# Kernel optimization log

Measured on AMD Instinct MI355X. Metric: run time of the kernel, lower is better.

The kernel has to match this reference:

```python
import jax, jax.numpy as jnp
import numpy as np

B, D = 4096, 1024
N_CLASSES = 100
INF = jnp.float32(3.4e38)


def setup_inputs() -> dict:
    key = jax.random.key(0)
    k1, k2 = jax.random.split(key)
    x = jax.random.normal(k1, (B, 1, D), dtype=jnp.float32)
    labels = jax.random.randint(k2, (B,), 0, N_CLASSES)
    return {"x": x, "labels": labels}


def _awareness_scan(xs, labels_f, R_init):
    # xs: [B, D] float32, labels_f: [B] float32
    b, d = xs.shape
    slots = jnp.arange(b)

    def step(state, inp):
        refs, ref_labels, n_refs, count, min_d, max_d, R = state
        xi, li = inp
        mask = slots < n_refs  # active reference slots
        # distances from candidate to current reference set (torch.cdist, p=2)
        d_all = jnp.sqrt(jnp.sum((refs - xi[None, :]) ** 2, axis=-1))  # [B]
        d_all = jax.lax.stop_gradient(d_all)
        d_act = jnp.where(mask, d_all, INF)
        min_act = jnp.min(d_act)
        is_first = count == 1
        # new reference iff ALL active distances exceed R (i.e. min > R)
        insert = is_first | (min_act > R)
        refs2 = jnp.where(insert, refs.at[n_refs].set(xi), refs)
        ref_labels2 = jnp.where(insert, ref_labels.at[n_refs].set(li), ref_labels)
        n_refs2 = n_refs + insert.astype(n_refs.dtype)
        # dynamic ray update (skipped on the very first sample, as in torch)
        max_act = jnp.max(jnp.where(mask, d_all, -INF))
        min_d2 = jnp.where(is_first, min_d, jnp.minimum(min_d, min_act))
        max_d2 = jnp.where(is_first, max_d, jnp.maximum(max_d, max_act))
        R2 = jnp.where(is_first, R, (min_d2 + max_d2) / 3)
        # prediction: nearest reference AFTER potential insertion
        mask2 = slots < n_refs2
        d2 = jnp.sqrt(jnp.sum((refs2 - xi[None, :]) ** 2, axis=-1))
        d2 = jax.lax.stop_gradient(d2)
        idx = jnp.argmin(jnp.where(mask2, d2, INF))
        pred = ref_labels2[idx]
        new_state = (refs2, ref_labels2, n_refs2, count + 1, min_d2, max_d2, R2)
        return new_state, pred

    init = (
        jnp.zeros((b, d), jnp.float32),   # reference instances buffer
        jnp.zeros((b,), jnp.float32),     # reference labels buffer
        jnp.int32(0),                     # n_refs
        jnp.int32(1),                     # count (starts at 1, as in torch)
        INF,                              # min_dist
        jnp.float32(0.0),                 # max_dist
        jnp.float32(R_init),              # R
    )
    _, preds = jax.lax.scan(step, init, (xs, labels_f))
    return preds  # [B] float32


def reference(x, labels):
    # x: [B, 1, D]; labels: [B] int. update_ref_insts=True, set_labels=labels.
    xs = x.reshape(x.shape[0], x.shape[2])
    labels_f = labels.astype(jnp.float32)
    return _awareness_scan(xs, labels_f, 1.0)
```

## Files before the change

### kernel.cpp

```cpp
#include <hip/hip_runtime.h>
#include <stdint.h>

#define B_N   4096
#define D_DIM 1024
#define INF_F 3.4e38f

typedef float floatx4 __attribute__((ext_vector_type(4)));

#define XQ_OFF 131072

__global__ __launch_bounds__(256)
void k_prep(const float* __restrict__ x, unsigned char* __restrict__ xq,
            float* __restrict__ norms,
            unsigned long long* __restrict__ minpack,
            unsigned int* __restrict__ maxbits) {
    const int row = blockIdx.x;
    const int t   = threadIdx.x;
    float4 v = ((const float4*)x)[row * 256 + t];
    int p = __builtin_amdgcn_cvt_pk_fp8_f32(v.x, v.y, 0, false);
    p     = __builtin_amdgcn_cvt_pk_fp8_f32(v.z, v.w, p, true);
    ((int*)xq)[row * 256 + t] = p;
    float s = v.x * v.x + v.y * v.y + v.z * v.z + v.w * v.w;
    #pragma unroll
    for (int off = 32; off; off >>= 1) s += __shfl_down(s, off);
    __shared__ float ws4[4];
    if ((t & 63) == 0) ws4[t >> 6] = s;
    __syncthreads();
    if (t == 0) {
        norms[row]   = ws4[0] + ws4[1] + ws4[2] + ws4[3];
        minpack[row] = 0xFFFFFFFFFFFFFFFFull;
        maxbits[row] = 0u;
    }
}

#define GLDS(g, l)                                                              \
    __builtin_amdgcn_global_load_lds(                                           \
        (__attribute__((address_space(1))) void*)(void*)(g),                    \
        (__attribute__((address_space(3))) void*)(void*)(l), 16, 0, 0)

__global__ __launch_bounds__(256, 3)
void k_pass1_fp8(const unsigned char* __restrict__ xq,
                 const float* __restrict__ norms,
                 unsigned long long* __restrict__ minpack,
                 unsigned int* __restrict__ maxbits) {
    int bid = blockIdx.x;
    int ti  = (int)((sqrtf(8.f * bid + 1.f) - 1.f) * 0.5f);
    while ((ti + 1) * (ti + 2) / 2 <= bid) ti++;
    while (ti * (ti + 1) / 2 > bid) ti--;
    int tj  = bid - ti * (ti + 1) / 2;

    __shared__ unsigned char As[16384];
    __shared__ unsigned char Bs[16384];
    __shared__ unsigned long long redMin[128][2];
    __shared__ float redMax[128][2];

    const int t    = threadIdx.x;
    const int w    = t >> 6, lane = t & 63;
    const int wm   = w >> 1, wn = w & 1;
    const int q4   = lane >> 4, c15 = lane & 15;
    const int i0   = ti * 128, j0 = tj * 128;

    const int sr = lane >> 3;
    const int sc = (lane & 7) ^ (sr & 7);

    const unsigned char* gA[4]; const unsigned char* gB[4];
    unsigned char* lA[4]; unsigned char* lB[4];
    #pragma unroll
    for (int q = 0; q < 4; q++) {
        int e   = w * 4 + q;
        int row = e * 8 + sr;
        gA[q] = xq + (size_t)(i0 + row) * D_DIM + sc * 16;
        gB[q] = xq + (size_t)(j0 + row) * D_DIM + sc * 16;
        lA[q] = As + e * 1024;
        lB[q] = Bs + e * 1024;
    }

    const int r7 = c15 & 7;
    int oib[4];
    #pragma unroll
    for (int kk = 0; kk < 4; kk++) {
        int sl  = kk * 2 + (q4 >> 1);
        oib[kk] = (((sl ^ r7) << 4) | ((q4 & 1) << 3));
    }
    int rbA[4], rbB[4];
    #pragma unroll
    for (int st = 0; st < 4; st++) {
        rbA[st] = (wm * 64 + st * 16 + c15) * 128;
        rbB[st] = (wn * 64 + st * 16 + c15) * 128;
    }

    floatx4 acc[4][4];
    #pragma unroll
    for (int m = 0; m < 4; m++)
        #pragma unroll
        for (int n = 0; n < 4; n++)
            acc[m][n] = (floatx4){0.f, 0.f, 0.f, 0.f};

    for (int it = 0; it < 8; it++) {
        __syncthreads();
        #pragma unroll
        for (int q = 0; q < 4; q++) {
            GLDS(gA[q], lA[q]);
            GLDS(gB[q], lB[q]);
            gA[q] += 128; gB[q] += 128;
        }
        __syncthreads();
        #pragma unroll
        for (int kk = 0; kk < 4; kk++) {
            long long af[4], bfr[4];
            #pragma unroll
            for (int st = 0; st < 4; st++) {
                af[st]  = *(const long long*)(As + rbA[st] + oib[kk]);
                bfr[st] = *(const long long*)(Bs + rbB[st] + oib[kk]);
            }
            #pragma unroll
            for (int m = 0; m < 4; m++)
                #pragma unroll
                for (int n = 0; n < 4; n++)
                    acc[m][n] = __builtin_amdgcn_mfma_f32_16x16x32_fp8_fp8(
                        af[m], bfr[n], acc[m][n], 0, 0, 0);
        }
    }

    float nj[4];
    #pragma unroll
    for (int st = 0; st < 4; st++) nj[st] = norms[j0 + wn * 64 + st * 16 + c15];

    #pragma unroll
    for (int st_m = 0; st_m < 4; st_m++) {
        #pragma unroll
        for (int r = 0; r < 4; r++) {
            int i_loc = wm * 64 + st_m * 16 + q4 * 4 + r;
            int gi    = i0 + i_loc;
            float ni  = norms[gi];
            unsigned long long mp = 0xFFFFFFFFFFFFFFFFull;
            float mx = -INF_F;
            #pragma unroll
            for (int st_n = 0; st_n < 4; st_n++) {
                int gj = j0 + wn * 64 + st_n * 16 + c15;
                if (gj < gi) {
                    float dot = acc[st_m][st_n][r];
                    float d   = sqrtf(fmaxf(ni + nj[st_n] - 2.f * dot, 0.f));
                    unsigned long long p =
                        ((unsigned long long)__float_as_uint(d) << 32) | (unsigned)gj;
                    if (p < mp) mp = p;
                    mx = fmaxf(mx, d);
                }
            }
            #pragma unroll
            for (int off = 1; off < 16; off <<= 1) {
                unsigned long long op = __shfl_xor(mp, off, 64);
                if (op < mp) mp = op;
                float om = __shfl_xor(mx, off, 64);
                mx = fmaxf(mx, om);
            }
            if (c15 == 0) { redMin[i_loc][wn] = mp; redMax[i_loc][wn] = mx; }
        }
    }
    __syncthreads();
    if (t < 128) {
        unsigned long long mp = redMin[t][0];
        if (redMin[t][1] < mp) mp = redMin[t][1];
        float mx = fmaxf(redMax[t][0], redMax[t][1]);
        if (mp != 0xFFFFFFFFFFFFFFFFull) {
            atomicMin(&minpack[i0 + t], mp);
            atomicMax(&maxbits[i0 + t], __float_as_uint(mx));
        }
    }
}

__global__ __launch_bounds__(1024)
void k_tail(const unsigned long long* __restrict__ minpack,
            const unsigned int* __restrict__ maxbits,
            const float* __restrict__ x, const float* __restrict__ norms,
            const int* __restrict__ labels, int* __restrict__ ref_idx,
            float* __restrict__ out) {
    const int t = threadIdx.x;
    float m[4], M[4];
    #pragma unroll
    for (int q = 0; q < 4; q++) {
        int i = t * 4 + q;
        unsigned long long p = minpack[i];
        float dmin = (p == 0xFFFFFFFFFFFFFFFFull)
                       ? INF_F : __uint_as_float((unsigned)(p >> 32));
        m[q] = (i == 0) ? INF_F : dmin;
        M[q] = (i == 0) ? -INF_F : __uint_as_float(maxbits[i]);
    }
    float pmin[4], pmax[4];
    pmin[0] = m[0]; pmax[0] = M[0];
    #pragma unroll
    for (int q = 1; q < 4; q++) {
        pmin[q] = fminf(pmin[q - 1], m[q]);
        pmax[q] = fmaxf(pmax[q - 1], M[q]);
    }
    __shared__ float smin[1024], smax[1024];
    smin[t] = pmin[3]; smax[t] = pmax[3];
    __syncthreads();
    for (int off = 1; off < 1024; off <<= 1) {
        float a = (t >= off) ? smin[t - off] : INF_F;
        float b = (t >= off) ? smax[t - off] : -INF_F;
        __syncthreads();
        smin[t] = fminf(smin[t], a);
        smax[t] = fmaxf(smax[t], b);
        __syncthreads();
    }
    float exMin = (t > 0) ? smin[t - 1] : INF_F;
    float exMax = (t > 0) ? smax[t - 1] : -INF_F;

    int viol = B_N;
    #pragma unroll
    for (int q = 0; q < 4; q++) {
        int i = t * 4 + q;
        if (i >= 1) {
            float pm = (q == 0) ? exMin : fminf(exMin, pmin[q - 1]);
            float pM = (q == 0) ? exMax : fmaxf(exMax, pmax[q - 1]);
            float R  = (i == 1) ? 1.0f : (pm + pM) / 3.0f;
            if (!(m[q] > R) && i < viol) viol = i;
        }
    }
    __shared__ int sv[1024];
    sv[t] = viol;
    __syncthreads();
    for (int off = 512; off; off >>= 1) {
        if (t < off) sv[t] = min(sv[t], sv[t + off]);
        __syncthreads();
    }
    const int s_star = sv[0];

    for (int i = t; i < s_star; i += 1024) out[i] = (float)labels[i];

    __shared__ float s_state[3];
    __shared__ int s_n;
    if (s_star < B_N && t == (s_star >> 2)) {
        int q = s_star & 3;
        float pm = (q == 0) ? exMin : fminf(exMin, pmin[q - 1]);
        float pM = (q == 0) ? exMax : fmaxf(exMax, pmax[q - 1]);
        float md = fminf(pm, m[q]);
        float Md = fmaxf(pM, M[q]);
        s_state[0] = md; s_state[1] = Md; s_state[2] = (md + Md) / 3.0f;
        s_n = s_star;
        unsigned long long p = minpack[s_star];
        int j = (int)(unsigned)(p & 0xFFFFFFFFu);
        out[s_star] = (float)labels[j];
    }
    if (s_star >= B_N) return;

    for (int s = t; s < s_star; s += 1024) ref_idx[s] = s;
    __syncthreads();

    __shared__ unsigned long long redp[1024];
    __shared__ float redm[1024];
    for (int i = s_star + 1; i < B_N; i++) {
        int n = s_n;
        const float* xi = x + (size_t)i * D_DIM;
        float ni = norms[i];
        unsigned long long mp = 0xFFFFFFFFFFFFFFFFull;
        float mx = -INF_F;
        for (int slot = t; slot < n; slot += 1024) {
            int j = ref_idx[slot];
            const float* xj = x + (size_t)j * D_DIM;
            float dot = 0.f;
            for (int k = 0; k < D_DIM; k++) dot = fmaf(xi[k], xj[k], dot);
            float d = sqrtf(fmaxf(ni + norms[j] - 2.f * dot, 0.f));
            unsigned long long p =
                ((unsigned long long)__float_as_uint(d) << 32) | (unsigned)slot;
            if (p < mp) mp = p;
            mx = fmaxf(mx, d);
        }
        redp[t] = mp; redm[t] = mx;
        __syncthreads();
        for (int off = 512; off; off >>= 1) {
            if (t < off) {
                if (redp[t + off] < redp[t]) redp[t] = redp[t + off];
                redm[t] = fmaxf(redm[t], redm[t + off]);
            }
            __syncthreads();
        }
        if (t == 0) {
            unsigned long long p = redp[0];
            float min_act = __uint_as_float((unsigned)(p >> 32));
            int minslot   = (int)(unsigned)(p & 0xFFFFFFFFu);
            float max_act = redm[0];
            bool insert = (min_act > s_state[2]);
            int pred;
            if (insert) {
                ref_idx[n] = i;
                s_n = n + 1;
                pred = (min_act <= 0.0f) ? labels[ref_idx[minslot]] : labels[i];
            } else {
                pred = labels[ref_idx[minslot]];
            }
            float md = fminf(s_state[0], min_act);
            float Md = fmaxf(s_state[1], max_act);
            s_state[0] = md; s_state[1] = Md; s_state[2] = (md + Md) / 3.0f;
            out[i] = (float)pred;
        }
        __syncthreads();
    }
}

extern "C" void kernel_launch(void* const* d_in, const int* in_sizes, int n_in,
                              void* d_out, int out_size, void* d_ws, size_t ws_size,
                              hipStream_t stream) {
    const float* x      = (const float*)d_in[0];
    const int*   labels = (const int*)d_in[1];
    float*       out    = (float*)d_out;
    char* ws = (char*)d_ws;
    unsigned long long* minpack = (unsigned long long*)ws;
    unsigned int*       maxbits = (unsigned int*)(ws + 32768);
    float*              norms   = (float*)(ws + 49152);
    int*                ref_idx = (int*)(ws + 65600);
    unsigned char*      xq      = (unsigned char*)(ws + XQ_OFF);

    k_prep<<<B_N, 256, 0, stream>>>(x, xq, norms, minpack, maxbits);
    const int ntiles  = B_N / 128;
    const int nblocks = ntiles * (ntiles + 1) / 2;
    k_pass1_fp8<<<nblocks, 256, 0, stream>>>(xq, norms, minpack, maxbits);
    k_tail<<<1, 1024, 0, stream>>>(minpack, maxbits, x, norms, labels, ref_idx, out);
}
```

Before: 102.3 us.

## Use 64x64 triangular tiles with split-K across two waves and LDS reduction

Shrinks the pairwise-distance GEMM tile from 128x128 with 4 waves to 64x64 with 2 waves, each wave computing half of the K dimension. Partial accumulators are then summed through LDS, and wave 0 does the epilogue with direct atomics. Each wave owns a private LDS region, so the per-iteration block barriers are replaced by a vmcnt wait. This gives about four times as many blocks for better CU occupancy and load balance. In exchange, each block reuses loaded data less and issues more global atomics.

```diff
diff --git a/kernel.cpp b/kernel.cpp
--- a/kernel.cpp
+++ b/kernel.cpp
@@ -4,6 +4,8 @@
 #define B_N   4096
 #define D_DIM 1024
 #define INF_F 3.4e38f
+#define NT    64
+#define NBLK  (NT * (NT + 1) / 2)
 
 typedef float floatx4 __attribute__((ext_vector_type(4)));
 
@@ -38,56 +40,47 @@
         (__attribute__((address_space(1))) void*)(void*)(g),                    \
         (__attribute__((address_space(3))) void*)(void*)(l), 16, 0, 0)
 
-__global__ __launch_bounds__(256, 3)
-void k_pass1_fp8(const unsigned char* __restrict__ xq,
-                 const float* __restrict__ norms,
-                 unsigned long long* __restrict__ minpack,
-                 unsigned int* __restrict__ maxbits) {
+__global__ __launch_bounds__(128, 3)
+void k_pass1(const unsigned char* __restrict__ xq,
+             const float* __restrict__ norms,
+             unsigned long long* __restrict__ minpack,
+             unsigned int* __restrict__ maxbits) {
     int bid = blockIdx.x;
     int ti  = (int)((sqrtf(8.f * bid + 1.f) - 1.f) * 0.5f);
     while ((ti + 1) * (ti + 2) / 2 <= bid) ti++;
     while (ti * (ti + 1) / 2 > bid) ti--;
     int tj  = bid - ti * (ti + 1) / 2;
 
-    __shared__ unsigned char As[16384];
-    __shared__ unsigned char Bs[16384];
-    __shared__ unsigned long long redMin[128][2];
-    __shared__ float redMax[128][2];
+    __shared__ __align__(16) unsigned char lds[16384];
 
     const int t    = threadIdx.x;
     const int w    = t >> 6, lane = t & 63;
-    const int wm   = w >> 1, wn = w & 1;
     const int q4   = lane >> 4, c15 = lane & 15;
-    const int i0   = ti * 128, j0 = tj * 128;
-
-    const int sr = lane >> 3;
-    const int sc = (lane & 7) ^ (sr & 7);
+    const int i0   = ti * 64, j0 = tj * 64;
+
+    unsigned char* myA = lds + w * 8192;
+    unsigned char* myB = myA + 4096;
+
+    const int sr = lane >> 2;
+    const int sc = (lane & 3) ^ (sr & 3);
 
     const unsigned char* gA[4]; const unsigned char* gB[4];
-    unsigned char* lA[4]; unsigned char* lB[4];
-    #pragma unroll
-    for (int q = 0; q < 4; q++) {
-        int e   = w * 4 + q;
-        int row = e * 8 + sr;
-        gA[q] = xq + (size_t)(i0 + row) * D_DIM + sc * 16;
-        gB[q] = xq + (size_t)(j0 + row) * D_DIM + sc * 16;
-        lA[q] = As + e * 1024;
-        lB[q] = Bs + e * 1024;
-    }
-
-    const int r7 = c15 & 7;
-    int oib[4];
-    #pragma unroll
-    for (int kk = 0; kk < 4; kk++) {
-        int sl  = kk * 2 + (q4 >> 1);
-        oib[kk] = (((sl ^ r7) << 4) | ((q4 & 1) << 3));
-    }
-    int rbA[4], rbB[4];
-    #pragma unroll
-    for (int st = 0; st < 4; st++) {
-        rbA[st] = (wm * 64 + st * 16 + c15) * 128;
-        rbB[st] = (wn * 64 + st * 16 + c15) * 128;
-    }
+    #pragma unroll
+    for (int e = 0; e < 4; e++) {
+        int row = e * 16 + sr;
+        size_t ko = (size_t)w * 512 + (size_t)sc * 16;
+        gA[e] = xq + (size_t)(i0 + row) * D_DIM + ko;
+        gB[e] = xq + (size_t)(j0 + row) * D_DIM + ko;
+    }
+
+    int foff[4][2];
+    #pragma unroll
+    for (int st = 0; st < 4; st++)
+        #pragma unroll
+        for (int kk = 0; kk < 2; kk++)
+            foff[st][kk] = (st * 16 + c15) * 64 +
+                           ((((kk << 1) | (q4 >> 1)) ^ (c15 & 3)) << 4) +
+                           ((q4 & 1) << 3);
 
     floatx4 acc[4][4];
     #pragma unroll
@@ -97,21 +90,20 @@
             acc[m][n] = (floatx4){0.f, 0.f, 0.f, 0.f};
 
     for (int it = 0; it < 8; it++) {
-        __syncthreads();
-        #pragma unroll
-        for (int q = 0; q < 4; q++) {
-            GLDS(gA[q], lA[q]);
-            GLDS(gB[q], lB[q]);
-            gA[q] += 128; gB[q] += 128;
-        }
-        __syncthreads();
-        #pragma unroll
-        for (int kk = 0; kk < 4; kk++) {
+        #pragma unroll
+        for (int e = 0; e < 4; e++) {
+            GLDS(gA[e], myA + e * 1024);
+            GLDS(gB[e], myB + e * 1024);
+            gA[e] += 64; gB[e] += 64;
+        }
+        asm volatile("s_waitcnt vmcnt(0)" ::: "memory");
+        #pragma unroll
+        for (int kk = 0; kk < 2; kk++) {
             long long af[4], bfr[4];
             #pragma unroll
             for (int st = 0; st < 4; st++) {
-                af[st]  = *(const long long*)(As + rbA[st] + oib[kk]);
-                bfr[st] = *(const long long*)(Bs + rbB[st] + oib[kk]);
+                af[st]  = *(const long long*)(myA + foff[st][kk]);
+                bfr[st] = *(const long long*)(myB + foff[st][kk]);
             }
             #pragma unroll
             for (int m = 0; m < 4; m++)
@@ -122,49 +114,61 @@
         }
     }
 
-    float nj[4];
-    #pragma unroll
-    for (int st = 0; st < 4; st++) nj[st] = norms[j0 + wn * 64 + st * 16 + c15];
-
-    #pragma unroll
-    for (int st_m = 0; st_m < 4; st_m++) {
-        #pragma unroll
-        for (int r = 0; r < 4; r++) {
-            int i_loc = wm * 64 + st_m * 16 + q4 * 4 + r;
-            int gi    = i0 + i_loc;
-            float ni  = norms[gi];
-            unsigned long long mp = 0xFFFFFFFFFFFFFFFFull;
-            float mx = -INF_F;
-            #pragma unroll
-            for (int st_n = 0; st_n < 4; st_n++) {
-                int gj = j0 + wn * 64 + st_n * 16 + c15;
-                if (gj < gi) {
-                    float dot = acc[st_m][st_n][r];
-                    float d   = sqrtf(fmaxf(ni + nj[st_n] - 2.f * dot, 0.f));
-                    unsigned long long p =
-                        ((unsigned long long)__float_as_uint(d) << 32) | (unsigned)gj;
-                    if (p < mp) mp = p;
-                    mx = fmaxf(mx, d);
+    __syncthreads();
+    float* cbuf = (float*)lds;
+    if (w == 1) {
+        #pragma unroll
+        for (int m = 0; m < 4; m++)
+            #pragma unroll
+            for (int n = 0; n < 4; n++)
+                #pragma unroll
+                for (int r = 0; r < 4; r++)
+                    cbuf[((m * 4 + n) * 4 + r) * 64 + lane] = acc[m][n][r];
+    }
+    __syncthreads();
+    if (w == 0) {
+        #pragma unroll
+        for (int m = 0; m < 4; m++)
+            #pragma unroll
+            for (int n = 0; n < 4; n++)
+                #pragma unroll
+                for (int r = 0; r < 4; r++)
+                    acc[m][n][r] += cbuf[((m * 4 + n) * 4 + r) * 64 + lane];
+
+        float njv[4];
+        #pragma unroll
+        for (int n = 0; n < 4; n++) njv[n] = norms[j0 + n * 16 + c15];
+        #pragma unroll
+        for (int m = 0; m < 4; m++) {
+            #pragma unroll
+            for (int r = 0; r < 4; r++) {
+                int gi   = i0 + m * 16 + q4 * 4 + r;
+                float ni = norms[gi];
+                unsigned long long mp = 0xFFFFFFFFFFFFFFFFull;
+                float mx = -INF_F;
+                #pragma unroll
+                for (int n = 0; n < 4; n++) {
+                    int gj = j0 + n * 16 + c15;
+                    if (gj < gi) {
+                        float d = sqrtf(fmaxf(ni + njv[n] - 2.f * acc[m][n][r], 0.f));
+                        unsigned long long p =
+                            ((unsigned long long)__float_as_uint(d) << 32) | (unsigned)gj;
+                        if (p < mp) mp = p;
+                        mx = fmaxf(mx, d);
+                    }
+                }
+                #pragma unroll
+                for (int off = 1; off < 16; off <<= 1) {
+                    unsigned long long op = __shfl_xor(mp, off, 64);
+                    if (op < mp) mp = op;
+                    float om = __shfl_xor(mx, off, 64);
+                    mx = fmaxf(mx, om);
+                }
+                if (c15 == 0 && mp != 0xFFFFFFFFFFFFFFFFull) {
+                    atomicMin(&minpack[gi], mp);
+                    atomicMax(&maxbits[gi], __float_as_uint(mx));
                 }
             }
-            #pragma unroll
-            for (int off = 1; off < 16; off <<= 1) {
-                unsigned long long op = __shfl_xor(mp, off, 64);
-                if (op < mp) mp = op;
-                float om = __shfl_xor(mx, off, 64);
-                mx = fmaxf(mx, om);
-            }
-            if (c15 == 0) { redMin[i_loc][wn] = mp; redMax[i_loc][wn] = mx; }
-        }
-    }
-    __syncthreads();
-    if (t < 128) {
-        unsigned long long mp = redMin[t][0];
-        if (redMin[t][1] < mp) mp = redMin[t][1];
-        float mx = fmaxf(redMax[t][0], redMax[t][1]);
-        if (mp != 0xFFFFFFFFFFFFFFFFull) {
-            atomicMin(&minpack[i0 + t], mp);
-            atomicMax(&maxbits[i0 + t], __float_as_uint(mx));
         }
     }
 }
@@ -313,8 +317,6 @@
     unsigned char*      xq      = (unsigned char*)(ws + XQ_OFF);
 
     k_prep<<<B_N, 256, 0, stream>>>(x, xq, norms, minpack, maxbits);
-    const int ntiles  = B_N / 128;
-    const int nblocks = ntiles * (ntiles + 1) / 2;
-    k_pass1_fp8<<<nblocks, 256, 0, stream>>>(xq, norms, minpack, maxbits);
+    k_pass1<<<NBLK, 128, 0, stream>>>(xq, norms, minpack, maxbits);
     k_tail<<<1, 1024, 0, stream>>>(minpack, maxbits, x, norms, labels, ref_idx, out);
 }
```

After: 111.6 us. +9.2%, slower.

## Double-buffer FP8 GEMM LDS tiles with halved K-chunk prefetch

Applied to the files above, without the earlier changes.

The pairwise-distance FP8 MFMA kernel now keeps two LDS buffers per operand, each holding a 64-byte K chunk. While the current chunk is being computed, the async global-to-LDS load of the next chunk is issued, so each iteration needs one barrier instead of two. The LDS swizzle and fragment offsets are recomputed for the narrower 64-byte rows. The aim is to hide global load latency behind MFMA work. In exchange there are twice as many loop iterations, each carrying less data.

```diff
diff --git a/kernel.cpp b/kernel.cpp
--- a/kernel.cpp
+++ b/kernel.cpp
@@ -49,8 +49,8 @@
     while (ti * (ti + 1) / 2 > bid) ti--;
     int tj  = bid - ti * (ti + 1) / 2;
 
-    __shared__ unsigned char As[16384];
-    __shared__ unsigned char Bs[16384];
+    __shared__ __align__(16) unsigned char As[2][8192];
+    __shared__ __align__(16) unsigned char Bs[2][8192];
     __shared__ unsigned long long redMin[128][2];
     __shared__ float redMax[128][2];
 
@@ -60,34 +60,28 @@
     const int q4   = lane >> 4, c15 = lane & 15;
     const int i0   = ti * 128, j0 = tj * 128;
 
-    const int sr = lane >> 3;
-    const int sc = (lane & 7) ^ (sr & 7);
-
-    const unsigned char* gA[4]; const unsigned char* gB[4];
-    unsigned char* lA[4]; unsigned char* lB[4];
-    #pragma unroll
-    for (int q = 0; q < 4; q++) {
-        int e   = w * 4 + q;
-        int row = e * 8 + sr;
-        gA[q] = xq + (size_t)(i0 + row) * D_DIM + sc * 16;
-        gB[q] = xq + (size_t)(j0 + row) * D_DIM + sc * 16;
-        lA[q] = As + e * 1024;
-        lB[q] = Bs + e * 1024;
-    }
-
-    const int r7 = c15 & 7;
-    int oib[4];
-    #pragma unroll
-    for (int kk = 0; kk < 4; kk++) {
-        int sl  = kk * 2 + (q4 >> 1);
-        oib[kk] = (((sl ^ r7) << 4) | ((q4 & 1) << 3));
-    }
-    int rbA[4], rbB[4];
-    #pragma unroll
-    for (int st = 0; st < 4; st++) {
-        rbA[st] = (wm * 64 + st * 16 + c15) * 128;
-        rbB[st] = (wn * 64 + st * 16 + c15) * 128;
-    }
+    const int sr = lane >> 2;
+    const int sc = (lane & 3) ^ (sr & 3);
+
+    const unsigned char* gA[2]; const unsigned char* gB[2];
+    int eoff[2];
+    #pragma unroll
+    for (int q = 0; q < 2; q++) {
+        int e   = w * 2 + q;
+        int row = e * 16 + sr;
+        gA[q]   = xq + (size_t)(i0 + row) * D_DIM + sc * 16;
+        gB[q]   = xq + (size_t)(j0 + row) * D_DIM + sc * 16;
+        eoff[q] = e * 1024;
+    }
+
+    int foff[4][2];
+    #pragma unroll
+    for (int st = 0; st < 4; st++)
+        #pragma unroll
+        for (int kk = 0; kk < 2; kk++)
+            foff[st][kk] = (st * 16 + c15) * 64 +
+                           ((((kk << 1) | (q4 >> 1)) ^ (c15 & 3)) << 4) +
+                           ((q4 & 1) << 3);
 
     floatx4 acc[4][4];
     #pragma unroll
@@ -96,22 +90,31 @@
         for (int n = 0; n < 4; n++)
             acc[m][n] = (floatx4){0.f, 0.f, 0.f, 0.f};
 
-    for (int it = 0; it < 8; it++) {
-        __syncthreads();
+    #pragma unroll
+    for (int q = 0; q < 2; q++) {
+        GLDS(gA[q], &As[0][eoff[q]]);
+        GLDS(gB[q], &Bs[0][eoff[q]]);
+    }
+
+    for (int it = 0; it < 16; it++) {
+        __syncthreads();
+        if (it < 15) {
+            const int nb = (it + 1) & 1;
+            #pragma unroll
+            for (int q = 0; q < 2; q++) {
+                GLDS(gA[q] + (it + 1) * 64, &As[nb][eoff[q]]);
+                GLDS(gB[q] + (it + 1) * 64, &Bs[nb][eoff[q]]);
+            }
+        }
+        const unsigned char* Ac = As[it & 1];
+        const unsigned char* Bc = Bs[it & 1];
         #pragma unroll
-        for (int q = 0; q < 4; q++) {
-            GLDS(gA[q], lA[q]);
-            GLDS(gB[q], lB[q]);
-            gA[q] += 128; gB[q] += 128;
-        }
-        __syncthreads();
-        #pragma unroll
-        for (int kk = 0; kk < 4; kk++) {
+        for (int kk = 0; kk < 2; kk++) {
             long long af[4], bfr[4];
             #pragma unroll
             for (int st = 0; st < 4; st++) {
-                af[st]  = *(const long long*)(As + rbA[st] + oib[kk]);
-                bfr[st] = *(const long long*)(Bs + rbB[st] + oib[kk]);
+                af[st]  = *(const long long*)(Ac + (wm * 64) * 64 + foff[st][kk]);
+                bfr[st] = *(const long long*)(Bc + (wn * 64) * 64 + foff[st][kk]);
             }
             #pragma unroll
             for (int m = 0; m < 4; m++)
```

Measured after the change: 109.4 us. 6.9% more time.
